# Kernel optimization log

Hardware: AMD Instinct MI355X
Metric: run time of the kernel (lower is better)

## Reference

```python
import jax, jax.numpy as jnp
import numpy as np
from jax import lax

KERNELS = (3, 5, 7, 9, 11, 13, 15)
H = W = 4096


def _box_mean(x, k):
    """2D box-mean filter with replicate (edge) padding, computed separably.

    Edge padding is separable, so (pad2d -> kxk box) == (padH -> kx1 box -> padW -> 1xk box).
    x: [N, 1, H, W]
    """
    p = k // 2
    kh = jnp.full((1, 1, k, 1), 1.0 / k, dtype=x.dtype)
    kw = jnp.full((1, 1, 1, k), 1.0 / k, dtype=x.dtype)
    dn = ('NCHW', 'OIHW', 'NCHW')
    y = jnp.pad(x, ((0, 0), (0, 0), (p, p), (0, 0)), mode='edge')
    y = lax.conv_general_dilated(y, kh, (1, 1), 'VALID', dimension_numbers=dn)
    y = jnp.pad(y, ((0, 0), (0, 0), (0, 0), (p, p)), mode='edge')
    y = lax.conv_general_dilated(y, kw, (1, 1), 'VALID', dimension_numbers=dn)
    return y


def setup_inputs() -> dict:
    key = jax.random.key(0)
    k1, k2 = jax.random.split(key)
    x = jax.random.uniform(k1, (1, 1, H, W), dtype=jnp.float32)
    # binary occupancy-style map, as float (torch uses mapU8 -> fp16 multiply)
    map_mask = (jax.random.uniform(k2, (H, W)) > 0.5).astype(jnp.float32)
    return {"x": x, "map_mask": map_mask}


def reference(x, map_mask):
    # sum of 7 multi-scale box means, averaged, then masked by the map
    acc = _box_mean(x, KERNELS[0])
    for k in KERNELS[1:]:
        acc = acc + _box_mean(x, k)
    out = acc / len(KERNELS)
    return out * map_mask[None, None, :, :]
```

## Files before the change

### kernel.cpp

```cpp
#include <hip/hip_runtime.h>


#define TILE   64
#define HALO   7
#define LHX    8
#define NCOL   80
#define NROW   78
#define PSTR   83
#define PROWSA 81
#define HH     4096
#define WW     4096

__global__ __launch_bounds__(256) void meanconv_kernel(
    const float* __restrict__ x, const float* __restrict__ mask,
    float* __restrict__ out)
{
    __shared__ float P[PROWSA * PSTR];
    const int tid = threadIdx.x;
    const int c0  = blockIdx.x * TILE;
    const int r0  = blockIdx.y * TILE;

    if (tid < 81) P[tid] = 0.0f;

    const bool xint = (c0 >= LHX) && (c0 - LHX + NCOL <= WW);

    for (int idx = tid; idx < NROW * 4; idx += 256) {
        const int lr  = idx >> 2;
        const int s   = idx & 3;
        const int gr  = min(max(r0 + lr - HALO, 0), HH - 1);
        const int gc0 = c0 - LHX + 20 * s;
        float v[20];
        if (xint) {
            const float* src = &x[(size_t)gr * WW + gc0];
            #pragma unroll
            for (int q = 0; q < 5; ++q) {
                const float4 t = *(const float4*)(src + 4 * q);
                v[4*q+0] = t.x; v[4*q+1] = t.y; v[4*q+2] = t.z; v[4*q+3] = t.w;
            }
        } else {
            #pragma unroll
            for (int i = 0; i < 20; ++i) {
                const int gc = min(max(gc0 + i, 0), WW - 1);
                v[i] = x[(size_t)gr * WW + gc];
            }
        }
        #pragma unroll
        for (int i = 1; i < 20; ++i) v[i] += v[i - 1];
        const float tot = v[19];
        float sum = tot;
        float u = __shfl_up(sum, 1, 4); if (s >= 1) sum += u;
        u       = __shfl_up(sum, 2, 4); if (s >= 2) sum += u;
        const float off = sum - tot;
        float* dst = &P[(lr + 1) * PSTR + 1 + 20 * s];
        #pragma unroll
        for (int i = 0; i < 20; ++i) dst[i] = v[i] + off;
    }
    __syncthreads();

    for (int idx = tid; idx < 80 * 4; idx += 256) {
        const int c  = (idx >> 2) + 1;
        const int s  = idx & 3;
        const int rs = 1 + 20 * s;
        float v[20];
        float run = 0.0f;
        #pragma unroll
        for (int i = 0; i < 20; ++i) {
            const int r = rs + i;
            float t = P[r * PSTR + c];
            t = (r < 79) ? t : 0.0f;
            run += t; v[i] = run;
        }
        const float tot = run;
        float sum = tot;
        float u = __shfl_up(sum, 1, 4); if (s >= 1) sum += u;
        u       = __shfl_up(sum, 2, 4); if (s >= 2) sum += u;
        const float off = sum - tot;
        #pragma unroll
        for (int i = 0; i < 20; ++i) {
            const int r = rs + i;
            if (r < 79) P[r * PSTR + c] = v[i] + off;
        }
    }
    __syncthreads();

    const int g  = tid & 3;
    const int ty = tid >> 2;
    const int B0 = 16 * g;
    const int A  = ty + HALO;
    float a[16];
    #pragma unroll
    for (int i = 0; i < 16; ++i) a[i] = 0.0f;

    #pragma unroll
    for (int p = 1; p <= 7; ++p) {
        const int   k = 2 * p + 1;
        const float w = 1.0f / (7.0f * (float)(k * k));
        const int   W = 17 + 2 * p;
        const float* rT = &P[(A - p)     * PSTR + B0 + LHX - p];
        const float* rB = &P[(A + p + 1) * PSTR + B0 + LHX - p];
        float D[31];
        #pragma unroll
        for (int q = 0; q < W; ++q) D[q] = rB[q] - rT[q];
        #pragma unroll
        for (int i = 0; i < 16; ++i)
            a[i] += w * (D[k + i] - D[i]);
    }

    const int gr = r0 + ty, gc = c0 + B0;
    const float* mrow = &mask[(size_t)gr * WW + gc];
    float*       orow = &out[(size_t)gr * WW + gc];
    #pragma unroll
    for (int q = 0; q < 4; ++q) {
        const float4 m = *(const float4*)(mrow + 4 * q);
        float4 o;
        o.x = a[4*q+0] * m.x;
        o.y = a[4*q+1] * m.y;
        o.z = a[4*q+2] * m.z;
        o.w = a[4*q+3] * m.w;
        *(float4*)(orow + 4 * q) = o;
    }
}

extern "C" void kernel_launch(void* const* d_in, const int* in_sizes, int n_in,
                              void* d_out, int out_size, void* d_ws, size_t ws_size,
                              hipStream_t stream) {
    const float* x    = (const float*)d_in[0];
    const float* mask = (const float*)d_in[1];
    float*       out  = (float*)d_out;
    dim3 grid(WW / TILE, HH / TILE);
    meanconv_kernel<<<grid, 256, 0, stream>>>(x, mask, out);
}
```

Measured before the change: 184.3 us.

## Process two row tiles per block and prefetch next tile's input into registers

Each block now handles two vertically stacked 64x64 tiles instead of one, halving the grid. While the first tile's box sums are computed, the global loads for the second tile's first 256 row segments are issued into registers, and mask loads are hoisted ahead of the arithmetic. The aim is to hide global load latency behind shared-memory compute. In exchange the block does more serial work, register pressure rises, an extra barrier is added per tile, and the halo rows are still reloaded for each tile.

Measured after the change: 194.1 us. +5.3%, slower.

```diff
diff --git a/kernel.cpp b/kernel.cpp
--- a/kernel.cpp
+++ b/kernel.cpp
@@ -16,20 +16,19 @@
     float* __restrict__ out)
 {
     __shared__ float P[PROWSA * PSTR];
-    const int tid = threadIdx.x;
-    const int c0  = blockIdx.x * TILE;
-    const int r0  = blockIdx.y * TILE;
+    const int tid    = threadIdx.x;
+    const int c0     = blockIdx.x * TILE;
+    const int r0base = blockIdx.y * (2 * TILE);
 
     if (tid < 81) P[tid] = 0.0f;
 
     const bool xint = (c0 >= LHX) && (c0 - LHX + NCOL <= WW);
 
-    for (int idx = tid; idx < NROW * 4; idx += 256) {
+    auto load_seg = [&](int r0, int idx, float* v) {
         const int lr  = idx >> 2;
         const int s   = idx & 3;
         const int gr  = min(max(r0 + lr - HALO, 0), HH - 1);
         const int gc0 = c0 - LHX + 20 * s;
-        float v[20];
         if (xint) {
             const float* src = &x[(size_t)gr * WW + gc0];
             #pragma unroll
@@ -44,6 +43,10 @@
                 v[i] = x[(size_t)gr * WW + gc];
             }
         }
+    };
+    auto prefix_write = [&](int idx, float* v) {
+        const int lr = idx >> 2;
+        const int s  = idx & 3;
         #pragma unroll
         for (int i = 1; i < 20; ++i) v[i] += v[i - 1];
         const float tot = v[19];
@@ -54,70 +57,93 @@
         float* dst = &P[(lr + 1) * PSTR + 1 + 20 * s];
         #pragma unroll
         for (int i = 0; i < 20; ++i) dst[i] = v[i] + off;
-    }
-    __syncthreads();
-
-    for (int idx = tid; idx < 80 * 4; idx += 256) {
-        const int c  = (idx >> 2) + 1;
-        const int s  = idx & 3;
-        const int rs = 1 + 20 * s;
-        float v[20];
-        float run = 0.0f;
-        #pragma unroll
-        for (int i = 0; i < 20; ++i) {
-            const int r = rs + i;
-            float t = P[r * PSTR + c];
-            t = (r < 79) ? t : 0.0f;
-            run += t; v[i] = run;
-        }
-        const float tot = run;
-        float sum = tot;
-        float u = __shfl_up(sum, 1, 4); if (s >= 1) sum += u;
-        u       = __shfl_up(sum, 2, 4); if (s >= 2) sum += u;
-        const float off = sum - tot;
-        #pragma unroll
-        for (int i = 0; i < 20; ++i) {
-            const int r = rs + i;
-            if (r < 79) P[r * PSTR + c] = v[i] + off;
-        }
-    }
-    __syncthreads();
+    };
 
     const int g  = tid & 3;
     const int ty = tid >> 2;
     const int B0 = 16 * g;
     const int A  = ty + HALO;
-    float a[16];
-    #pragma unroll
-    for (int i = 0; i < 16; ++i) a[i] = 0.0f;
+
+    float v[20];
+    load_seg(r0base, tid, v);
 
     #pragma unroll
-    for (int p = 1; p <= 7; ++p) {
-        const int   k = 2 * p + 1;
-        const float w = 1.0f / (7.0f * (float)(k * k));
-        const int   W = 17 + 2 * p;
-        const float* rT = &P[(A - p)     * PSTR + B0 + LHX - p];
-        const float* rB = &P[(A + p + 1) * PSTR + B0 + LHX - p];
-        float D[31];
+    for (int t = 0; t < 2; ++t) {
+        const int r0 = r0base + TILE * t;
+
+        prefix_write(tid, v);
+        if (tid < 56) {
+            float w2[20];
+            load_seg(r0, tid + 256, w2);
+            prefix_write(tid + 256, w2);
+        }
+        __syncthreads();
+
+        for (int idx = tid; idx < 80 * 4; idx += 256) {
+            const int c  = (idx >> 2) + 1;
+            const int s  = idx & 3;
+            const int rs = 1 + 20 * s;
+            float vv[20];
+            float run = 0.0f;
+            #pragma unroll
+            for (int i = 0; i < 20; ++i) {
+                const int r = rs + i;
+                float tt = P[r * PSTR + c];
+                tt = (r < 79) ? tt : 0.0f;
+                run += tt; vv[i] = run;
+            }
+            const float tot = run;
+            float sum = tot;
+            float u = __shfl_up(sum, 1, 4); if (s >= 1) sum += u;
+            u       = __shfl_up(sum, 2, 4); if (s >= 2) sum += u;
+            const float off = sum - tot;
+            #pragma unroll
+            for (int i = 0; i < 20; ++i) {
+                const int r = rs + i;
+                if (r < 79) P[r * PSTR + c] = vv[i] + off;
+            }
+        }
+        __syncthreads();
+
+        if (t == 0) load_seg(r0base + TILE, tid, v);
+
+        const int gr = r0 + ty, gc = c0 + B0;
+        const float* mrow = &mask[(size_t)gr * WW + gc];
+        const float4 m0 = *(const float4*)(mrow);
+        const float4 m1 = *(const float4*)(mrow + 4);
+        const float4 m2 = *(const float4*)(mrow + 8);
+        const float4 m3 = *(const float4*)(mrow + 12);
+
+        float a[16];
         #pragma unroll
-        for (int q = 0; q < W; ++q) D[q] = rB[q] - rT[q];
+        for (int i = 0; i < 16; ++i) a[i] = 0.0f;
+
         #pragma unroll
-        for (int i = 0; i < 16; ++i)
-            a[i] += w * (D[k + i] - D[i]);
-    }
+        for (int p = 1; p <= 7; ++p) {
+            const int   k = 2 * p + 1;
+            const float wgt = 1.0f / (7.0f * (float)(k * k));
+            const int   W = 17 + 2 * p;
+            const float* rT = &P[(A - p)     * PSTR + B0 + LHX - p];
+            const float* rB = &P[(A + p + 1) * PSTR + B0 + LHX - p];
+            float D[31];
+            #pragma unroll
+            for (int q = 0; q < W; ++q) D[q] = rB[q] - rT[q];
+            #pragma unroll
+            for (int i = 0; i < 16; ++i)
+                a[i] += wgt * (D[k + i] - D[i]);
+        }
+        __syncthreads();
 
-    const int gr = r0 + ty, gc = c0 + B0;
-    const float* mrow = &mask[(size_t)gr * WW + gc];
-    float*       orow = &out[(size_t)gr * WW + gc];
-    #pragma unroll
-    for (int q = 0; q < 4; ++q) {
-        const float4 m = *(const float4*)(mrow + 4 * q);
+        float* orow = &out[(size_t)gr * WW + gc];
         float4 o;
-        o.x = a[4*q+0] * m.x;
-        o.y = a[4*q+1] * m.y;
-        o.z = a[4*q+2] * m.z;
-        o.w = a[4*q+3] * m.w;
-        *(float4*)(orow + 4 * q) = o;
+        o.x = a[0]*m0.x;  o.y = a[1]*m0.y;  o.z = a[2]*m0.z;  o.w = a[3]*m0.w;
+        *(float4*)(orow)      = o;
+        o.x = a[4]*m1.x;  o.y = a[5]*m1.y;  o.z = a[6]*m1.z;  o.w = a[7]*m1.w;
+        *(float4*)(orow + 4)  = o;
+        o.x = a[8]*m2.x;  o.y = a[9]*m2.y;  o.z = a[10]*m2.z; o.w = a[11]*m2.w;
+        *(float4*)(orow + 8)  = o;
+        o.x = a[12]*m3.x; o.y = a[13]*m3.y; o.z = a[14]*m3.z; o.w = a[15]*m3.w;
+        *(float4*)(orow + 12) = o;
     }
 }
 
@@ -127,6 +153,6 @@
     const float* x    = (const float*)d_in[0];
     const float* mask = (const float*)d_in[1];
     float*       out  = (float*)d_out;
-    dim3 grid(WW / TILE, HH / TILE);
+    dim3 grid(WW / TILE, HH / (2 * TILE));
     meanconv_kernel<<<grid, 256, 0, stream>>>(x, mask, out);
 }
```
